# Performance work log

Hardware: AMD Instinct MI355X
Metric: run time of the kernel (lower is better)

Reference implementation:

```python
import jax, jax.numpy as jnp
import numpy as np

B, T = 128, 1024
H1, H2 = 768, 768


def setup_inputs() -> dict:
    key = jax.random.key(0)
    ks = jax.random.split(key, 12)
    s1 = 1.0 / np.sqrt(H1)
    s2 = 1.0 / np.sqrt(H2)
    return {
        "x": jax.random.normal(ks[0], (B, 2, T), dtype=jnp.float32),
        "W_ih1": jax.random.uniform(ks[1], (H1, 2), jnp.float32, -s1, s1),
        "W_hh1": jax.random.uniform(ks[2], (H1, H1), jnp.float32, -s1, s1),
        "b_ih1": jax.random.uniform(ks[3], (H1,), jnp.float32, -s1, s1),
        "b_hh1": jax.random.uniform(ks[4], (H1,), jnp.float32, -s1, s1),
        "W_ih2": jax.random.uniform(ks[5], (H2, H1), jnp.float32, -s2, s2),
        "W_hh2": jax.random.uniform(ks[6], (H2, H2), jnp.float32, -s2, s2),
        "b_ih2": jax.random.uniform(ks[7], (H2,), jnp.float32, -s2, s2),
        "b_hh2": jax.random.uniform(ks[8], (H2,), jnp.float32, -s2, s2),
        "W_lin": jax.random.uniform(ks[9], (2, H2), jnp.float32, -s2, s2),
        "b_lin": jax.random.uniform(ks[10], (2,), jnp.float32, -s2, s2),
        "future": 0,
    }


def reference(x, W_ih1, W_hh1, b_ih1, b_hh1, W_ih2, W_hh2, b_ih2, b_hh2,
              W_lin, b_lin, future):
    Bb = x.shape[0]
    xs = jnp.transpose(x, (2, 0, 1))  # [T, B, 2]

    def cell(xt, ht, W_ih, W_hh, b_ih, b_hh):
        return jnp.tanh(xt @ W_ih.T + b_ih + ht @ W_hh.T + b_hh)

    def step(carry, xt):
        h1, h2 = carry
        h1 = cell(xt, h1, W_ih1, W_hh1, b_ih1, b_hh1)
        h2 = cell(h1, h2, W_ih2, W_hh2, b_ih2, b_hh2)
        out = h2 @ W_lin.T + b_lin  # [B, 2]
        return (h1, h2), out

    h1 = jnp.zeros((Bb, W_hh1.shape[0]), dtype=x.dtype)
    h2 = jnp.zeros((Bb, W_hh2.shape[0]), dtype=x.dtype)
    (h1, h2), outs = jax.lax.scan(step, (h1, h2), xs)  # outs: [T, B, 2]

    if future > 0:
        def fstep(carry, _):
            h1, h2, out = carry
            h1 = cell(out, h1, W_ih1, W_hh1, b_ih1, b_hh1)
            h2 = cell(h1, h2, W_ih2, W_hh2, b_ih2, b_hh2)
            out = h2 @ W_lin.T + b_lin
            return (h1, h2, out), out
        _, fouts = jax.lax.scan(fstep, (h1, h2, outs[-1]), None, length=future)
        outs = jnp.concatenate([outs, fouts], axis=0)

    return jnp.transpose(outs, (1, 2, 0))  # [B, 2, T+future]
```

## Files before the change

### kernel.cpp

```cpp
#include <hip/hip_runtime.h>
#include <math.h>


typedef short s16x8 __attribute__((ext_vector_type(8)));
typedef float fx4   __attribute__((ext_vector_type(4)));

#define NWG    256
#define T_LEN  1024
#define H      768
#define GROUPS 8
#define GROWS  16

#define MAP_OFF    0
#define KBR_OFF    1024
#define GRP_BASE   8192
#define G_FL1  0
#define G_FH2D 512
#define G_FP   2048
#define G_PB   3584
#define G_H1   28160
#define G_H2   421376
#define GRP_STRIDE 520704
#define HB_SZ 24576
#define WS_TOTAL (GRP_BASE + GROUPS * GRP_STRIDE)

__device__ __forceinline__ unsigned short f2bf(float x) {
    unsigned u = __float_as_uint(x);
    unsigned r = (u + 0x7FFFu + ((u >> 16) & 1u)) >> 16;
    return (unsigned short)r;
}
__device__ __forceinline__ float bf2f(unsigned short b) {
    return __uint_as_float(((unsigned)b) << 16);
}
__device__ __forceinline__ fx4 mfma16(s16x8 a, s16x8 b, fx4 c) {
    return __builtin_amdgcn_mfma_f32_16x16x32_bf16(a, b, c, 0, 0, 0);
}

__device__ __forceinline__ void st_ag(unsigned* p, unsigned v) {
    __hip_atomic_store(p, v, __ATOMIC_RELAXED, __HIP_MEMORY_SCOPE_AGENT);
}
__device__ __forceinline__ unsigned ld_ag(const unsigned* p) {
    return __hip_atomic_load(p, __ATOMIC_RELAXED, __HIP_MEMORY_SCOPE_AGENT);
}
__device__ __forceinline__ void acq_ag() {
    __builtin_amdgcn_fence(__ATOMIC_ACQUIRE, "agent");
}
__device__ __forceinline__ void st32_sc0(unsigned* p, unsigned v) {
    asm volatile("global_store_dword %0, %1, off sc0" :: "v"(p), "v"(v) : "memory");
}
__device__ __forceinline__ void stflag_l2(unsigned* p, unsigned v) {
    asm volatile("global_atomic_swap %0, %1, off" :: "v"(p), "v"(v) : "memory");
}
__device__ __forceinline__ unsigned rdflag_l2(unsigned* p) {
    unsigned v, z = 0;
    asm volatile("global_atomic_add %0, %1, %2, off sc0\n\ts_waitcnt vmcnt(0)"
                 : "=v"(v) : "v"(p), "v"(z) : "memory");
    return v;
}
__device__ __forceinline__ void inv_l1() {
    asm volatile("buffer_inv sc0" ::: "memory");
}

template<bool LOCAL> __device__ __forceinline__ unsigned rdp(unsigned* p) {
    if constexpr (LOCAL) return rdflag_l2(p); else return ld_ag(p);
}
template<bool LOCAL> __device__ __forceinline__ void std32(unsigned* p, unsigned v) {
    if constexpr (LOCAL) st32_sc0(p, v); else st_ag(p, v);
}

__device__ __forceinline__ void load_wfrag(const float* __restrict__ W,
                                           int col, int kk, s16x8& hi, s16x8& lo) {
    const float* p = W + (long)col * H + kk;
#pragma unroll
    for (int j = 0; j < 8; j++) {
        float w = p[j];
        unsigned short h = f2bf(w);
        float r = w - bf2f(h);
        hi[j] = (short)h;
        lo[j] = (short)f2bf(r);
    }
}

__device__ __forceinline__ void ld6(const unsigned short* p, s16x8 (&d)[6]) {
#pragma unroll
    for (int ks = 0; ks < 6; ks++)
        d[ks] = *reinterpret_cast<const s16x8*>(p + ks * 32);
}

__device__ __forceinline__ unsigned wave_min(unsigned v) {
#pragma unroll
    for (int o = 32; o; o >>= 1) {
        unsigned u = (unsigned)__shfl_xor((int)v, o);
        v = v < u ? v : u;
    }
    return v;
}

__device__ __forceinline__ unsigned wait_wv(unsigned* f, int n, unsigned T,
                                            int lane, unsigned cached) {
    if (cached >= T) return cached;
    unsigned m;
    long spin = 0;
    for (;;) {
        unsigned v = (lane < n) ? rdflag_l2(f + lane * 16) : 0xFFFFFFFFu;
        m = wave_min(v);
        if (m >= T) break;
        __builtin_amdgcn_s_sleep(1);
        if (++spin > (1L << 20)) break;
    }
    return m;
}

__device__ __forceinline__ unsigned gate_raw(unsigned* raw, int n, unsigned T,
                                             int tid, unsigned cached,
                                             volatile unsigned* sh) {
    if (cached >= T) return cached;
    if (tid < 64) {
        unsigned m;
        long spin = 0;
        for (;;) {
            unsigned v = (tid < n) ? rdflag_l2(raw + tid * 16) : 0xFFFFFFFFu;
            m = wave_min(v);
            if (m >= T) break;
            __builtin_amdgcn_s_sleep(1);
            if (++spin > (1L << 20)) break;
        }
        if (tid == 0) *sh = m;
    }
    __syncthreads();
    return *sh;
}

__device__ __forceinline__ void wait_agent(unsigned* f, int n, unsigned T,
                                           int tid, bool acquire) {
    if (tid < 64) {
        int l = tid < n ? tid : n - 1;
        long spin = 0;
        for (;;) {
            if (wave_min(ld_ag(f + l * 16)) >= T) break;
            __builtin_amdgcn_s_sleep(1);
            if (++spin > (1L << 20)) break;
        }
    }
    if (acquire && tid == 0) acq_ag();
    __syncthreads();
}

#define DRAIN() do { asm volatile("s_waitcnt vmcnt(0)" ::: "memory"); __syncthreads(); } while (0)

template<bool LOCAL>
__device__ __forceinline__ void run_group(
    int group, int lrank, int tid, int lane, int w, int l15, int lk8,
    const float* __restrict__ x,
    const float* __restrict__ Wih1, const float* __restrict__ Whh1,
    const float* __restrict__ bih1, const float* __restrict__ bhh1,
    const float* __restrict__ Wih2, const float* __restrict__ Whh2,
    const float* __restrict__ bih2, const float* __restrict__ bhh2,
    const float* __restrict__ Wlin, const float* __restrict__ blin,
    float* __restrict__ out, unsigned char* __restrict__ gb,
    float (*red)[16][97], volatile unsigned* shm)
{
    unsigned* fL1  = (unsigned*)(gb + G_FL1);
    unsigned* fH2d = (unsigned*)(gb + G_FH2D);
    unsigned* fP   = (unsigned*)(gb + G_FP);
    float*    Pb   = (float*)(gb + G_PB);
    const int kb0 = w * 192;

    if (lrank < 8) {
        const int c = lrank;
        const int col0 = c * 96;

        s16x8 whi[6][6], wlo[6][6];
#pragma unroll
        for (int ks = 0; ks < 6; ks++)
#pragma unroll
            for (int nt = 0; nt < 6; nt++)
                load_wfrag(Whh1, col0 + nt * 16 + l15, kb0 + ks * 32 + lk8,
                           whi[ks][nt], wlo[ks][nt]);

        const int er = tid >> 4;
        const int ec0 = (tid & 15) * 6;
        const int b = group * GROWS + er;
        float bs[6], wi0[6], wi1[6];
#pragma unroll
        for (int j = 0; j < 6; j++) {
            int cg = col0 + ec0 + j;
            bs[j] = bih1[cg] + bhh1[cg];
            wi0[j] = Wih1[cg * 2 + 0];
            wi1[j] = Wih1[cg * 2 + 1];
        }
        const int ov = tid >> 5;
        const int oj = tid & 31;
        const int orow = 2 * c + (ov >> 1);
        const int ooo = ov & 1;
        const float blv = blin[ooo];

        unsigned fpc = 0;
        unsigned fl1w = 0;

        for (int t = 0; t < T_LEN; t++) {
            const int rs = (t + 7) & 7;
            const int wsl = t & 7;
            float x0 = x[b * 2048 + t];
            float x1 = x[b * 2048 + 1024 + t];

            if (t >= 7) {
                if constexpr (LOCAL)
                    fpc = gate_raw(fP, 24, (unsigned)(t - 6), tid, fpc, &shm[0]);
                else
                    wait_agent(fP, 24, (unsigned)(t - 6), tid, false);
                if (tid < 128) {
                    float p = 0.f;
                    if (oj < 24)
                        p = __uint_as_float(rdp<LOCAL>((unsigned*)
                            (Pb + ((((t - 7) & 7) * 16 + orow) * 2 + ooo) * 24 + oj)));
#pragma unroll
                    for (int o = 16; o; o >>= 1) p += __shfl_down(p, o, 32);
                    if (oj == 0) out[(group * GROWS + orow) * 2048 + ooo * 1024 + (t - 7)] = p + blv;
                }
            }

            if (t) {
                if constexpr (LOCAL) {
                    fl1w = wait_wv(fL1 + 2 * w * 16, 2, (unsigned)t, lane, fl1w);
                    inv_l1();
                } else {
                    wait_agent(fL1, 8, (unsigned)t, tid, true);
                }
            }

            const unsigned short* Hh = (const unsigned short*)(gb + G_H1 + rs * 2 * HB_SZ);
            const unsigned short* Hl = (const unsigned short*)(gb + G_H1 + rs * 2 * HB_SZ + HB_SZ);
            s16x8 ah[6], al[6];
            ld6(Hh + l15 * H + kb0 + lk8, ah);
            ld6(Hl + l15 * H + kb0 + lk8, al);

            fx4 acc[6];
#pragma unroll
            for (int nt = 0; nt < 6; nt++) acc[nt] = fx4{0.f, 0.f, 0.f, 0.f};
#pragma unroll
            for (int ks = 0; ks < 6; ks++)
#pragma unroll
                for (int nt = 0; nt < 6; nt++) {
                    acc[nt] = mfma16(ah[ks], whi[ks][nt], acc[nt]);
                    acc[nt] = mfma16(ah[ks], wlo[ks][nt], acc[nt]);
                    acc[nt] = mfma16(al[ks], whi[ks][nt], acc[nt]);
                }

#pragma unroll
            for (int nt = 0; nt < 6; nt++)
#pragma unroll
                for (int i = 0; i < 4; i++)
                    red[w][(lane >> 4) * 4 + i][nt * 16 + l15] = acc[nt][i];
            __syncthreads();

            unsigned hw[3], lw[3];
#pragma unroll
            for (int jj = 0; jj < 3; jj++) {
                unsigned hp = 0, lp = 0;
#pragma unroll
                for (int k = 0; k < 2; k++) {
                    int j = jj * 2 + k;
                    int cc = ec0 + j;
                    float v = red[0][er][cc] + red[1][er][cc] + red[2][er][cc] + red[3][er][cc];
                    v += x0 * wi0[j] + x1 * wi1[j] + bs[j];
                    v = tanhf(v);
                    unsigned short hb = f2bf(v);
                    unsigned short lb = f2bf(v - bf2f(hb));
                    hp |= ((unsigned)hb) << (16 * k);
                    lp |= ((unsigned)lb) << (16 * k);
                }
                hw[jj] = hp; lw[jj] = lp;
            }

            unsigned* Dh = (unsigned*)(gb + G_H1 + wsl * 2 * HB_SZ) + ((long)er * H + col0 + ec0) / 2;
            unsigned* Dl = (unsigned*)(gb + G_H1 + wsl * 2 * HB_SZ + HB_SZ) + ((long)er * H + col0 + ec0) / 2;
            std32<LOCAL>(Dh + 0, hw[0]); std32<LOCAL>(Dh + 1, hw[1]); std32<LOCAL>(Dh + 2, hw[2]);
            std32<LOCAL>(Dl + 0, lw[0]); std32<LOCAL>(Dl + 1, lw[1]); std32<LOCAL>(Dl + 2, lw[2]);

            DRAIN();
            if (tid == 0) {
                if constexpr (LOCAL) stflag_l2(fL1 + c * 16, (unsigned)(t + 1));
                else st_ag(fL1 + c * 16, (unsigned)(t + 1));
            }
        }

        if constexpr (LOCAL)
            fpc = gate_raw(fP, 24, (unsigned)T_LEN, tid, fpc, &shm[0]);
        else
            wait_agent(fP, 24, (unsigned)T_LEN, tid, false);
        if (tid < 128) {
#pragma unroll
            for (int par = 0; par < 7; par++) {
                int tt = T_LEN - 7 + par;
                float p = 0.f;
                if (oj < 24)
                    p = __uint_as_float(rdp<LOCAL>((unsigned*)
                        (Pb + (((tt & 7) * 16 + orow) * 2 + ooo) * 24 + oj)));
#pragma unroll
                for (int o = 16; o; o >>= 1) p += __shfl_down(p, o, 32);
                if (oj == 0) out[(group * GROWS + orow) * 2048 + ooo * 1024 + tt] = p + blv;
            }
        }
    } else {
        const int q = lrank - 8;
        const int col0 = q * 32;

        s16x8 ghi[2][6], glo[2][6], ihi[2][6], ilo[2][6];
#pragma unroll
        for (int nt = 0; nt < 2; nt++)
#pragma unroll
            for (int ks = 0; ks < 6; ks++) {
                load_wfrag(Whh2, col0 + nt * 16 + l15, kb0 + ks * 32 + lk8, ghi[nt][ks], glo[nt][ks]);
                load_wfrag(Wih2, col0 + nt * 16 + l15, kb0 + ks * 32 + lk8, ihi[nt][ks], ilo[nt][ks]);
            }

        const int er = tid >> 4;
        const int ec0 = (tid & 15) * 2;
        const float bsA = bih2[col0 + ec0] + bhh2[col0 + ec0];
        const float bsB = bih2[col0 + ec0 + 1] + bhh2[col0 + ec0 + 1];

        const int ro = tid >> 1, oo = tid & 1;
        float wl[32];
        if (tid < 32) {
#pragma unroll
            for (int cc = 0; cc < 32; cc++) wl[cc] = Wlin[oo * H + col0 + cc];
        }

        unsigned fh2w = 0, fl1w = 0;

        for (int t = 0; t < T_LEN; t++) {
            const int rb = (t + 1) & 1;
            const int wb = t & 1;
            const int hs = t & 7;

            if (t) {
                if constexpr (LOCAL)
                    fh2w = wait_wv(fH2d + 6 * w * 16, 6, (unsigned)t, lane, fh2w);
                else
                    wait_agent(fH2d, 24, (unsigned)t, tid, true);
            }
            bool h1rdy = false;
            if constexpr (LOCAL) {
                inv_l1();
                h1rdy = (fl1w >= (unsigned)(t + 1));
            }

            const unsigned short* Gh = (const unsigned short*)(gb + G_H2 + rb * 2 * HB_SZ);
            const unsigned short* Gl = (const unsigned short*)(gb + G_H2 + rb * 2 * HB_SZ + HB_SZ);
            const unsigned short* Hh = (const unsigned short*)(gb + G_H1 + hs * 2 * HB_SZ);
            const unsigned short* Hl = (const unsigned short*)(gb + G_H1 + hs * 2 * HB_SZ + HB_SZ);

            s16x8 ah[6], al[6], bh[6], bl[6];
            ld6(Gh + l15 * H + kb0 + lk8, ah);
            ld6(Gl + l15 * H + kb0 + lk8, al);
            if (h1rdy) {
                ld6(Hh + l15 * H + kb0 + lk8, bh);
                ld6(Hl + l15 * H + kb0 + lk8, bl);
            }

            fx4 a2[2];
            a2[0] = fx4{0.f, 0.f, 0.f, 0.f};
            a2[1] = fx4{0.f, 0.f, 0.f, 0.f};
#pragma unroll
            for (int ks = 0; ks < 6; ks++)
#pragma unroll
                for (int nt = 0; nt < 2; nt++) {
                    a2[nt] = mfma16(ah[ks], ghi[nt][ks], a2[nt]);
                    a2[nt] = mfma16(ah[ks], glo[nt][ks], a2[nt]);
                    a2[nt] = mfma16(al[ks], ghi[nt][ks], a2[nt]);
                }

            if (!h1rdy) {
                if constexpr (LOCAL) {
                    fl1w = wait_wv(fL1 + 2 * w * 16, 2, (unsigned)(t + 1), lane, fl1w);
                } else {
                    wait_agent(fL1, 8, (unsigned)(t + 1), tid, true);
                }
                ld6(Hh + l15 * H + kb0 + lk8, bh);
                ld6(Hl + l15 * H + kb0 + lk8, bl);
            }

#pragma unroll
            for (int ks = 0; ks < 6; ks++)
#pragma unroll
                for (int nt = 0; nt < 2; nt++) {
                    a2[nt] = mfma16(bh[ks], ihi[nt][ks], a2[nt]);
                    a2[nt] = mfma16(bh[ks], ilo[nt][ks], a2[nt]);
                    a2[nt] = mfma16(bl[ks], ihi[nt][ks], a2[nt]);
                }

#pragma unroll
            for (int nt = 0; nt < 2; nt++)
#pragma unroll
                for (int i = 0; i < 4; i++)
                    red[w][(lane >> 4) * 4 + i][nt * 16 + l15] = a2[nt][i];
            __syncthreads();

            float v0 = red[0][er][ec0] + red[1][er][ec0] + red[2][er][ec0] + red[3][er][ec0] + bsA;
            float v1 = red[0][er][ec0 + 1] + red[1][er][ec0 + 1] + red[2][er][ec0 + 1] + red[3][er][ec0 + 1] + bsB;
            v0 = tanhf(v0); v1 = tanhf(v1);
            unsigned short hb0 = f2bf(v0), hb1 = f2bf(v1);
            unsigned hp = ((unsigned)hb0) | (((unsigned)hb1) << 16);
            unsigned lp = ((unsigned)f2bf(v0 - bf2f(hb0))) | (((unsigned)f2bf(v1 - bf2f(hb1))) << 16);
            unsigned* Dh = (unsigned*)(gb + G_H2 + wb * 2 * HB_SZ) + ((long)er * H + col0 + ec0) / 2;
            unsigned* Dl = (unsigned*)(gb + G_H2 + wb * 2 * HB_SZ + HB_SZ) + ((long)er * H + col0 + ec0) / 2;
            std32<LOCAL>(Dh, hp);
            std32<LOCAL>(Dl, lp);
            red[0][er][ec0] = v0;
            red[0][er][ec0 + 1] = v1;

            DRAIN();
            if (tid == 0) {
                if constexpr (LOCAL) stflag_l2(fH2d + q * 16, (unsigned)(t + 1));
                else st_ag(fH2d + q * 16, (unsigned)(t + 1));
            }

            if (tid < 32) {
                float s = 0.f;
#pragma unroll
                for (int cc = 0; cc < 32; cc++) s += red[0][ro][cc] * wl[cc];
                std32<LOCAL>((unsigned*)&Pb[(((t & 7) * 16 + ro) * 2 + oo) * 24 + q],
                             __float_as_uint(s));
            }

            DRAIN();
            if (tid == 0) {
                if constexpr (LOCAL) stflag_l2(fP + q * 16, (unsigned)(t + 1));
                else st_ag(fP + q * 16, (unsigned)(t + 1));
            }
        }
    }
}

__global__ __launch_bounds__(256, 1) void rnn_persist(
    const float* __restrict__ x,
    const float* __restrict__ Wih1, const float* __restrict__ Whh1,
    const float* __restrict__ bih1, const float* __restrict__ bhh1,
    const float* __restrict__ Wih2, const float* __restrict__ Whh2,
    const float* __restrict__ bih2, const float* __restrict__ bhh2,
    const float* __restrict__ Wlin, const float* __restrict__ blin,
    float* __restrict__ out, unsigned char* __restrict__ ws)
{
    const int wg = blockIdx.x;
    const int tid = threadIdx.x;
    const int lane = tid & 63;
    const int w = tid >> 6;
    const int l15 = lane & 15;
    const int lk8 = (lane >> 4) * 8;

    __shared__ float red[4][16][97];
    __shared__ int iscr[256];
    __shared__ unsigned shm[4];

    unsigned* map = (unsigned*)(ws + MAP_OFF);
    unsigned* kbr = (unsigned*)(ws + KBR_OFF);

    int key;
    asm volatile("s_getreg_b32 %0, hwreg(HW_REG_XCC_ID, 0, 4)" : "=s"(key));
    key &= 0xF;

    if (tid == 0) st_ag(map + wg, (unsigned)(key + 1));
    unsigned kj;
    {
        long spin = 0;
        for (;;) {
            kj = ld_ag(map + tid);
            if (kj) break;
            __builtin_amdgcn_s_sleep(2);
            if (++spin > (1L << 20)) break;
        }
    }
    int contrib = (((int)kj - 1) < key || (((int)kj - 1) == key && tid < wg)) ? 1 : 0;
    iscr[tid] = contrib;
    __syncthreads();
#pragma unroll
    for (int s = 128; s; s >>= 1) {
        if (tid < s) iscr[tid] += iscr[tid + s];
        __syncthreads();
    }
    const int rank = iscr[0];
    __syncthreads();
    const int group = rank >> 5, lrank = rank & 31;

    if (tid == 0) st_ag(kbr + rank, (unsigned)(key + 1));
    unsigned kv;
    {
        long spin = 0;
        for (;;) {
            kv = ld_ag(kbr + tid);
            if (kv) break;
            __builtin_amdgcn_s_sleep(2);
            if (++spin > (1L << 20)) break;
        }
    }
    int eq = ((int)kv - 1 == key) ? 1 : 0;
    int bad = ((tid >> 5) == group && !eq) ? 1 : 0;
    iscr[tid] = eq | (bad << 16);
    __syncthreads();
#pragma unroll
    for (int s = 128; s; s >>= 1) {
        if (tid < s) iscr[tid] += iscr[tid + s];
        __syncthreads();
    }
    const int r0 = iscr[0];
    __syncthreads();
    const bool local = ((r0 & 0xFFFF) == 32) && ((r0 >> 16) == 0);

    unsigned char* gb = ws + GRP_BASE + (size_t)group * GRP_STRIDE;

    if (local)
        run_group<true>(group, lrank, tid, lane, w, l15, lk8,
                        x, Wih1, Whh1, bih1, bhh1, Wih2, Whh2, bih2, bhh2,
                        Wlin, blin, out, gb, red, shm);
    else
        run_group<false>(group, lrank, tid, lane, w, l15, lk8,
                         x, Wih1, Whh1, bih1, bhh1, Wih2, Whh2, bih2, bhh2,
                         Wlin, blin, out, gb, red, shm);
}

extern "C" void kernel_launch(void* const* d_in, const int* in_sizes, int n_in,
                              void* d_out, int out_size, void* d_ws, size_t ws_size,
                              hipStream_t stream) {
    const float* x    = (const float*)d_in[0];
    const float* Wih1 = (const float*)d_in[1];
    const float* Whh1 = (const float*)d_in[2];
    const float* bih1 = (const float*)d_in[3];
    const float* bhh1 = (const float*)d_in[4];
    const float* Wih2 = (const float*)d_in[5];
    const float* Whh2 = (const float*)d_in[6];
    const float* bih2 = (const float*)d_in[7];
    const float* bhh2 = (const float*)d_in[8];
    const float* Wlin = (const float*)d_in[9];
    const float* blin = (const float*)d_in[10];

    hipMemsetAsync(d_ws, 0, WS_TOTAL, stream);

    rnn_persist<<<NWG, 256, 0, stream>>>(x, Wih1, Whh1, bih1, bhh1,
                                         Wih2, Whh2, bih2, bhh2,
                                         Wlin, blin, (float*)d_out,
                                         (unsigned char*)d_ws);
}
```

Measured before the change: 5.223 ms.

## Use per-wave h2 readiness flags and rotate the output projection across waves

```diff
diff --git a/kernel.cpp b/kernel.cpp
--- a/kernel.cpp
+++ b/kernel.cpp
@@ -16,11 +16,11 @@
 #define GRP_BASE   8192
 #define G_FL1  0
 #define G_FH2D 512
-#define G_FP   2048
-#define G_PB   3584
-#define G_H1   28160
-#define G_H2   421376
-#define GRP_STRIDE 520704
+#define G_FP   6656
+#define G_PB   8192
+#define G_H1   32768
+#define G_H2   425984
+#define GRP_STRIDE 524288
 #define HB_SZ 24576
 #define WS_TOTAL (GRP_BASE + GROUPS * GRP_STRIDE)
 
@@ -60,6 +60,7 @@
 __device__ __forceinline__ void inv_l1() {
     asm volatile("buffer_inv sc0" ::: "memory");
 }
+#define WAVE_VMCNT() asm volatile("s_waitcnt vmcnt(0)" ::: "memory")
 
 template<bool LOCAL> __device__ __forceinline__ unsigned rdp(unsigned* p) {
     if constexpr (LOCAL) return rdflag_l2(p); else return ld_ag(p);
@@ -134,10 +135,14 @@
 __device__ __forceinline__ void wait_agent(unsigned* f, int n, unsigned T,
                                            int tid, bool acquire) {
     if (tid < 64) {
-        int l = tid < n ? tid : n - 1;
         long spin = 0;
         for (;;) {
-            if (wave_min(ld_ag(f + l * 16)) >= T) break;
+            unsigned v = (tid < n) ? ld_ag(f + tid * 16) : 0xFFFFFFFFu;
+            if (tid + 64 < n) {
+                unsigned v2 = ld_ag(f + (tid + 64) * 16);
+                v = v < v2 ? v : v2;
+            }
+            if (wave_min(v) >= T) break;
             __builtin_amdgcn_s_sleep(1);
             if (++spin > (1L << 20)) break;
         }
@@ -320,9 +325,9 @@
         const float bsA = bih2[col0 + ec0] + bhh2[col0 + ec0];
         const float bsB = bih2[col0 + ec0 + 1] + bhh2[col0 + ec0 + 1];
 
-        const int ro = tid >> 1, oo = tid & 1;
+        const int ro = lane >> 1, oo = lane & 1;
         float wl[32];
-        if (tid < 32) {
+        if (lane < 32) {
 #pragma unroll
             for (int cc = 0; cc < 32; cc++) wl[cc] = Wlin[oo * H + col0 + cc];
         }
@@ -336,9 +341,9 @@
 
             if (t) {
                 if constexpr (LOCAL)
-                    fh2w = wait_wv(fH2d + 6 * w * 16, 6, (unsigned)t, lane, fh2w);
+                    fh2w = wait_wv(fH2d + 24 * w * 16, 24, (unsigned)t, lane, fh2w);
                 else
-                    wait_agent(fH2d, 24, (unsigned)t, tid, true);
+                    wait_agent(fH2d, 96, (unsigned)t, tid, true);
             }
             bool h1rdy = false;
             if constexpr (LOCAL) {
@@ -407,27 +412,43 @@
             unsigned* Dl = (unsigned*)(gb + G_H2 + wb * 2 * HB_SZ + HB_SZ) + ((long)er * H + col0 + ec0) / 2;
             std32<LOCAL>(Dh, hp);
             std32<LOCAL>(Dl, lp);
+
+            if constexpr (LOCAL) {
+                WAVE_VMCNT();
+                if (lane == 0) stflag_l2(fH2d + (q * 4 + w) * 16, (unsigned)(t + 1));
+            }
+
             red[0][er][ec0] = v0;
             red[0][er][ec0 + 1] = v1;
-
-            DRAIN();
-            if (tid == 0) {
-                if constexpr (LOCAL) stflag_l2(fH2d + q * 16, (unsigned)(t + 1));
-                else st_ag(fH2d + q * 16, (unsigned)(t + 1));
-            }
-
-            if (tid < 32) {
-                float s = 0.f;
-#pragma unroll
-                for (int cc = 0; cc < 32; cc++) s += red[0][ro][cc] * wl[cc];
-                std32<LOCAL>((unsigned*)&Pb[(((t & 7) * 16 + ro) * 2 + oo) * 24 + q],
-                             __float_as_uint(s));
-            }
-
-            DRAIN();
-            if (tid == 0) {
-                if constexpr (LOCAL) stflag_l2(fP + q * 16, (unsigned)(t + 1));
-                else st_ag(fP + q * 16, (unsigned)(t + 1));
+            __syncthreads();
+
+            if constexpr (LOCAL) {
+                if (w == (t & 3)) {
+                    if (lane < 32) {
+                        float s = 0.f;
+#pragma unroll
+                        for (int cc = 0; cc < 32; cc++) s += red[0][ro][cc] * wl[cc];
+                        st32_sc0((unsigned*)&Pb[(((t & 7) * 16 + ro) * 2 + oo) * 24 + q],
+                                 __float_as_uint(s));
+                    }
+                    WAVE_VMCNT();
+                    if (lane == 0) stflag_l2(fP + q * 16, (unsigned)(t + 1));
+                }
+            } else {
+                if (tid == 0) {
+#pragma unroll
+                    for (int i = 0; i < 4; i++)
+                        st_ag(fH2d + (q * 4 + i) * 16, (unsigned)(t + 1));
+                }
+                if (tid < 32) {
+                    float s = 0.f;
+#pragma unroll
+                    for (int cc = 0; cc < 32; cc++) s += red[0][tid >> 1][cc] * wl[cc];
+                    st_ag((unsigned*)&Pb[(((t & 7) * 16 + (tid >> 1)) * 2 + (tid & 1)) * 24 + q],
+                          __float_as_uint(s));
+                }
+                DRAIN();
+                if (tid == 0) st_ag(fP + q * 16, (unsigned)(t + 1));
             }
         }
     }
```

Result: no change. 5.286 ms (+1.2%).
